# Performance work log

Hardware: AMD Instinct MI355X
Metric: run time of the kernel (lower is better)

## Reference

```python
import jax, jax.numpy as jnp
import numpy as np

NUM_HEADS = 8
HEAD_DIM = 64
WIN = (8, 8, 8)  # (wT, wH, wW)


def setup_inputs() -> dict:
    key = jax.random.key(0)
    k1, k2, k3 = jax.random.split(key, 3)
    B, T, H, W, C = 2, 16, 32, 32, 512
    d_inner = NUM_HEADS * HEAD_DIM  # 512
    x = jax.random.normal(k1, (B, T * H * W, C), dtype=jnp.float32)
    # torch Linear weights stored transposed as [in, out] for y = x @ w
    w_qkv = jax.random.normal(k2, (C, 3 * d_inner), dtype=jnp.float32) * (C ** -0.5)
    w_proj = jax.random.normal(k3, (d_inner, C), dtype=jnp.float32) * (d_inner ** -0.5)
    b_proj = jnp.zeros((C,), dtype=jnp.float32)
    return {"x": x, "w_qkv": w_qkv, "w_proj": w_proj, "b_proj": b_proj,
            "T": T, "H": H, "W": W}


def reference(x, w_qkv, w_proj, b_proj, T, H, W):
    B, N, C = x.shape
    wT, wH, wW = WIN
    scale = HEAD_DIM ** -0.5
    # module re-derives T if N mismatches T*H*W
    if N != T * H * W:
        T = N // (H * W)
    xv = x.reshape(B, T, H, W, C)
    pt, ph, pw = (-T) % wT, (-H) % wH, (-W) % wW
    if pt or ph or pw:
        xv = jnp.pad(xv, ((0, 0), (0, pt), (0, ph), (0, pw), (0, 0)))
    Tp, Hp, Wp = T + pt, H + ph, W + pw
    nT, nH, nW = Tp // wT, Hp // wH, Wp // wW
    L = wT * wH * wW  # tokens per window
    # window partition: [B*nT*nH*nW, L, C]
    xw = xv.reshape(B, nT, wT, nH, wH, nW, wW, C)
    xw = xw.transpose(0, 1, 3, 5, 2, 4, 6, 7).reshape(-1, L, C)
    # qkv projection (no bias)
    qkv = xw @ w_qkv  # [nw, L, 3*nh*hd]
    q, k, v = jnp.split(qkv, 3, axis=-1)

    def heads(t):
        return t.reshape(t.shape[0], L, NUM_HEADS, HEAD_DIM).transpose(0, 2, 1, 3)

    q, k, v = heads(q), heads(k), heads(v)  # [nw, h, L, d]
    attn = jax.nn.softmax(jnp.einsum('nhid,nhjd->nhij', q, k) * scale, axis=-1)
    o = jnp.einsum('nhij,nhjd->nhid', attn, v)
    o = o.transpose(0, 2, 1, 3).reshape(-1, L, NUM_HEADS * HEAD_DIM)
    o = o @ w_proj + b_proj  # output projection
    # window un-partition
    o = o.reshape(B, nT, nH, nW, wT, wH, wW, C)
    o = o.transpose(0, 1, 4, 2, 5, 3, 6, 7).reshape(B, Tp, Hp, Wp, C)
    return o[:, :T, :H, :W].reshape(B, N, C)
```

## Files before the change

### kernel.cpp

```cpp
#include <hip/hip_runtime.h>
#include <hip/hip_bf16.h>

typedef __hip_bfloat16 bf16;
typedef __attribute__((ext_vector_type(8))) short bf16x8;
typedef __attribute__((ext_vector_type(4))) float f32x4;

#define MROWS 32768
#define CDIM 512
#define SEL_STRIDE (512*512*64)

__device__ __forceinline__ int win_to_src_row(int m) {
  int win = m >> 9, l = m & 511;
  int b = win >> 5, rr = win & 31;
  int nt = rr >> 4, nh = (rr >> 2) & 3, nw = rr & 3;
  int wt = l >> 6, wh = (l >> 3) & 7, ww = l & 7;
  int tt = nt * 8 + wt, hh = nh * 8 + wh, wp = nw * 8 + ww;
  return (b << 14) + (tt << 10) + (hh << 5) + wp;
}

__device__ __forceinline__ unsigned short bf16bits(bf16 h) {
  return __builtin_bit_cast(unsigned short, h);
}

__device__ __forceinline__ ushort4 pack4(f32x4 a) {
  ushort4 o;
  o.x = bf16bits(__float2bfloat16(a[0]));
  o.y = bf16bits(__float2bfloat16(a[1]));
  o.z = bf16bits(__float2bfloat16(a[2]));
  o.w = bf16bits(__float2bfloat16(a[3]));
  return o;
}

__device__ __forceinline__ int xcd_chunk(int bx, int n) {
  return (bx & 7) * (n >> 3) + (bx >> 3);
}

__global__ __launch_bounds__(256) void transpose_cvt_kernel(
    const float* __restrict__ src, bf16* __restrict__ dst, int R, int C) {
  __shared__ float tile[32][33];
  int bc = blockIdx.x * 32, br = blockIdx.y * 32;
  int tx = threadIdx.x, ty = threadIdx.y;
#pragma unroll
  for (int i = 0; i < 32; i += 8)
    tile[ty + i][tx] = src[(size_t)(br + ty + i) * C + bc + tx];
  __syncthreads();
#pragma unroll
  for (int i = 0; i < 32; i += 8)
    dst[(size_t)(bc + ty + i) * R + br + tx] = __float2bfloat16(tile[tx][ty + i]);
}

__global__ __launch_bounds__(256) void perm_x_kernel(const float* __restrict__ x,
                                                     bf16* __restrict__ xw) {
  const int total = MROWS * (CDIM / 4);
  for (int i = blockIdx.x * 256 + threadIdx.x; i < total; i += 2048 * 256) {
    int m = i >> 7, c4 = (i & 127) * 4;
    int src = win_to_src_row(m);
    float4 v = *(const float4*)(x + (size_t)src * CDIM + c4);
    ushort4 o;
    o.x = bf16bits(__float2bfloat16(v.x));
    o.y = bf16bits(__float2bfloat16(v.y));
    o.z = bf16bits(__float2bfloat16(v.z));
    o.w = bf16bits(__float2bfloat16(v.w));
    *(ushort4*)(xw + (size_t)m * CDIM + c4) = o;
  }
}

#define BM 128
#define BN 128
#define BK 64

__device__ __forceinline__ void gload16(const bf16* g, const bf16* l) {
  __builtin_amdgcn_global_load_lds(
      (const __attribute__((address_space(1))) unsigned int*)g,
      (__attribute__((address_space(3))) unsigned int*)l, 16, 0, 0);
}

template <int MODE, int SWAP>
__global__ __launch_bounds__(256) void gemm_bt_kernel(
    const bf16* __restrict__ A, const bf16* __restrict__ Bt, int Ntiles, int bn0,
    bf16* __restrict__ qkv_out, float* __restrict__ out,
    const float* __restrict__ bias) {
  __shared__ __align__(16) bf16 Asl[BM * BK];
  __shared__ __align__(16) bf16 Bsl[BN * BK];
  const int K = 512;
  int l2 = xcd_chunk(blockIdx.x, gridDim.x);
  int bn = bn0 + (l2 >> 3) % Ntiles;
  int bm = (l2 & 7) + (l2 / (8 * Ntiles)) * 8;
  int t = threadIdx.x, lane = t & 63, w = t >> 6;
  int wr = w >> 1, wc = w & 1;
  int l15 = lane & 15, lh = lane >> 4;
  f32x4 acc[4][4] = {};

  for (int kt = 0; kt < K; kt += BK) {
    __syncthreads();
#pragma unroll
    for (int i = 0; i < 4; ++i) {
      int f = i * 256 + t;
      int row = f >> 3, cb = f & 7;
      gload16(A + (size_t)(bm * BM + row) * K + kt + cb * 8,
              &Asl[(i * 256 + w * 64) * 8]);
    }
#pragma unroll
    for (int i = 0; i < 4; ++i) {
      int f = i * 256 + t;
      int row = f >> 3, cb = f & 7;
      gload16(Bt + (size_t)(bn * BN + row) * K + kt + cb * 8,
              &Bsl[(i * 256 + w * 64) * 8]);
    }
    __syncthreads();
#pragma unroll
    for (int kk = 0; kk < 2; ++kk) {
      bf16x8 af[4], bfr[4];
#pragma unroll
      for (int mi = 0; mi < 4; ++mi)
        af[mi] = *(const bf16x8*)&Asl[(wr * 64 + mi * 16 + l15) * BK + kk * 32 + lh * 8];
#pragma unroll
      for (int nj = 0; nj < 4; ++nj)
        bfr[nj] = *(const bf16x8*)&Bsl[(wc * 64 + nj * 16 + l15) * BK + kk * 32 + lh * 8];
#pragma unroll
      for (int mi = 0; mi < 4; ++mi)
#pragma unroll
        for (int nj = 0; nj < 4; ++nj) {
          if (SWAP)
            acc[mi][nj] = __builtin_amdgcn_mfma_f32_16x16x32_bf16(
                bfr[nj], af[mi], acc[mi][nj], 0, 0, 0);
          else
            acc[mi][nj] = __builtin_amdgcn_mfma_f32_16x16x32_bf16(
                af[mi], bfr[nj], acc[mi][nj], 0, 0, 0);
        }
    }
  }

  if (MODE == 0 && SWAP == 1) {
#pragma unroll
    for (int mi = 0; mi < 4; ++mi) {
      int tok_g = bm * BM + wr * 64 + mi * 16 + l15;
      int win = tok_g >> 9, tk = tok_g & 511;
#pragma unroll
      for (int nj = 0; nj < 4; ++nj) {
        int c = bn * BN + wc * 64 + nj * 16 + lh * 4;
        int sel = c >> 9, cc = c & 511;
        int head = cc >> 6, d0 = cc & 63;
        *(ushort4*)(qkv_out + (size_t)sel * SEL_STRIDE +
                    (((size_t)(win * 8 + head)) * 512 + tk) * 64 + d0) =
            pack4(acc[mi][nj]);
      }
    }
  } else if (MODE == 0) {
#pragma unroll
    for (int mi = 0; mi < 4; ++mi) {
      int tok0 = bm * BM + wr * 64 + mi * 16 + lh * 4;
      int win = tok0 >> 9, tk0 = tok0 & 511;
#pragma unroll
      for (int nj = 0; nj < 4; ++nj) {
        int cc = (bn - 8) * BN + wc * 64 + nj * 16 + l15;
        int head = cc >> 6, d = cc & 63;
        *(ushort4*)(qkv_out + 2 * (size_t)SEL_STRIDE +
                    (((size_t)(win * 8 + head)) * 64 + d) * 512 + tk0) =
            pack4(acc[mi][nj]);
      }
    }
  } else {
#pragma unroll
    for (int mi = 0; mi < 4; ++mi) {
      int row = bm * BM + wr * 64 + mi * 16 + lh * 4;
#pragma unroll
      for (int r = 0; r < 4; ++r) {
        int srow = win_to_src_row(row + r);
        float* op = out + (size_t)srow * CDIM;
#pragma unroll
        for (int nj = 0; nj < 4; ++nj) {
          int col = bn * BN + wc * 64 + nj * 16 + l15;
          op[col] = acc[mi][nj][r] + bias[col];
        }
      }
    }
  }
}

__global__ __launch_bounds__(256, 2) void attn_kernel(const bf16* __restrict__ qkv_ws,
                                                      bf16* __restrict__ o_ws) {
  __shared__ __align__(16) bf16 Pl[4][4][16 * 64];
  int l2 = xcd_chunk(blockIdx.x, 1024);
  int wh = l2 >> 1, qc = l2 & 1;
  int win = wh >> 3, head = wh & 7;
  int t = threadIdx.x, lane = t & 63, w = t >> 6;
  int l15 = lane & 15, lh = lane >> 4;
  const bf16* qb = qkv_ws + (size_t)wh * (512 * 64);
  const bf16* kb = qb + SEL_STRIDE;
  const bf16* vtb = qkv_ws + 2 * (size_t)SEL_STRIDE + (size_t)wh * (64 * 512);

  const float c_scale = 0.18033688011112042f;
  int q0 = qc * 256 + w * 64;
  bf16x8 qf[4][2];
#pragma unroll
  for (int qi = 0; qi < 4; ++qi)
#pragma unroll
    for (int kk = 0; kk < 2; ++kk)
      qf[qi][kk] = *(const bf16x8*)(qb + (size_t)(q0 + qi * 16 + l15) * 64 + kk * 32 + lh * 8);

  f32x4 acco[4][4] = {};
  float lsum[4][4] = {};
  for (int kt = 0; kt < 8; ++kt) {
    bf16x8 kf[4][2], vf[4][2];
#pragma unroll
    for (int kj = 0; kj < 4; ++kj) {
      int tok = kt * 64 + kj * 16 + l15;
#pragma unroll
      for (int kk = 0; kk < 2; ++kk)
        kf[kj][kk] = *(const bf16x8*)(kb + (size_t)tok * 64 + kk * 32 + lh * 8);
    }
#pragma unroll
    for (int nj = 0; nj < 4; ++nj) {
      int d = nj * 16 + l15;
#pragma unroll
      for (int kk = 0; kk < 2; ++kk)
        vf[nj][kk] = *(const bf16x8*)(vtb + (size_t)d * 512 + kt * 64 + kk * 32 + lh * 8);
    }
#pragma unroll
    for (int qi = 0; qi < 4; ++qi) {
      f32x4 s[4] = {};
#pragma unroll
      for (int kj = 0; kj < 4; ++kj)
#pragma unroll
        for (int kk = 0; kk < 2; ++kk)
          s[kj] = __builtin_amdgcn_mfma_f32_16x16x32_bf16(qf[qi][kk], kf[kj][kk], s[kj], 0, 0, 0);
#pragma unroll
      for (int kj = 0; kj < 4; ++kj)
#pragma unroll
        for (int r = 0; r < 4; ++r) {
          float p = __builtin_exp2f(s[kj][r] * c_scale);
          s[kj][r] = p;
          lsum[qi][r] += p;
        }
      char* myP = (char*)&Pl[w][qi][0];
#pragma unroll
      for (int kj = 0; kj < 4; ++kj)
#pragma unroll
        for (int r = 0; r < 4; ++r) {
          int prow = lh * 4 + r, pcol = kj * 16 + l15;
          *(bf16*)(myP + prow * 128 + ((pcol * 2) ^ ((prow & 7) << 4))) =
              __float2bfloat16(s[kj][r]);
        }
      bf16x8 pa[2];
#pragma unroll
      for (int kk = 0; kk < 2; ++kk)
        pa[kk] = *(const bf16x8*)(myP + l15 * 128 + ((kk * 64 + lh * 16) ^ ((l15 & 7) << 4)));
#pragma unroll
      for (int nj = 0; nj < 4; ++nj)
#pragma unroll
        for (int kk = 0; kk < 2; ++kk)
          acco[qi][nj] = __builtin_amdgcn_mfma_f32_16x16x32_bf16(pa[kk], vf[nj][kk],
                                                                 acco[qi][nj], 0, 0, 0);
    }
  }
#pragma unroll
  for (int qi = 0; qi < 4; ++qi) {
    float inv[4];
#pragma unroll
    for (int r = 0; r < 4; ++r) {
      float v = lsum[qi][r];
      v += __shfl_xor(v, 1);
      v += __shfl_xor(v, 2);
      v += __shfl_xor(v, 4);
      v += __shfl_xor(v, 8);
      inv[r] = __frcp_rn(v);
    }
#pragma unroll
    for (int nj = 0; nj < 4; ++nj)
#pragma unroll
      for (int r = 0; r < 4; ++r) {
        int row = q0 + qi * 16 + lh * 4 + r;
        int d = nj * 16 + l15;
        o_ws[((size_t)win * 512 + row) * 512 + head * 64 + d] =
            __float2bfloat16(acco[qi][nj][r] * inv[r]);
      }
  }
}

extern "C" void kernel_launch(void* const* d_in, const int* in_sizes, int n_in,
                              void* d_out, int out_size, void* d_ws, size_t ws_size,
                              hipStream_t stream) {
  const float* x = (const float*)d_in[0];
  const float* w_qkv = (const float*)d_in[1];
  const float* w_proj = (const float*)d_in[2];
  const float* b_proj = (const float*)d_in[3];
  float* out = (float*)d_out;

  const size_t OFF_QKV = 33554432;
  const size_t OFF_WQ = OFF_QKV + 100663296;
  const size_t OFF_WP = OFF_WQ + 1572864;
  const size_t NEED = OFF_WP + 524288;
  if (ws_size < NEED) return;

  char* ws = (char*)d_ws;
  bf16* xw = (bf16*)ws;
  bf16* qkv = (bf16*)(ws + OFF_QKV);
  bf16* wqkvT = (bf16*)(ws + OFF_WQ);
  bf16* wprojT = (bf16*)(ws + OFF_WP);
  bf16* o_ws = xw;

  transpose_cvt_kernel<<<dim3(1536 / 32, 512 / 32), dim3(32, 8), 0, stream>>>(w_qkv, wqkvT, 512, 1536);
  transpose_cvt_kernel<<<dim3(512 / 32, 512 / 32), dim3(32, 8), 0, stream>>>(w_proj, wprojT, 512, 512);
  perm_x_kernel<<<2048, 256, 0, stream>>>(x, xw);
  gemm_bt_kernel<0, 1><<<256 * 8, 256, 0, stream>>>(xw, wqkvT, 8, 0, qkv, nullptr, nullptr);
  gemm_bt_kernel<0, 0><<<256 * 4, 256, 0, stream>>>(xw, wqkvT, 4, 8, qkv, nullptr, nullptr);
  attn_kernel<<<1024, 256, 0, stream>>>(qkv, o_ws);
  gemm_bt_kernel<1, 0><<<256 * 4, 256, 0, stream>>>(o_ws, wprojT, 4, 0, nullptr, out, b_proj);
}
```

Measured before the change: 240.1 us.

## Keep attention probabilities in registers, merge QKV GEMM launches, vectorize projection stores

The attention kernel now computes S transposed (K as the A operand) in 32-key chunks. It packs the probabilities to bf16 with v_cvt_pk_bf16_f32 and rearranges them across lanes with ds_bpermute, replacing the LDS round trip for P. The per-row softmax sum is reduced with fewer shuffles. The two QKV GEMM launches are merged into one launch of 12 column tiles, with a runtime branch choosing the operand order and epilogue. The output projection is switched to the swapped layout so it can write float4 rows and load bias as vectors. This adds permute instructions and a divergence-free runtime branch in the GEMM, and halves the key-chunk size, which creates more loop iterations.

New measurement: 237.7 us. About the same (-1.0%).

```diff
diff --git a/kernel.cpp b/kernel.cpp
--- a/kernel.cpp
+++ b/kernel.cpp
@@ -4,6 +4,7 @@
 typedef __hip_bfloat16 bf16;
 typedef __attribute__((ext_vector_type(8))) short bf16x8;
 typedef __attribute__((ext_vector_type(4))) float f32x4;
+typedef __attribute__((ext_vector_type(4))) unsigned int u32x4;
 
 #define MROWS 32768
 #define CDIM 512
@@ -29,6 +30,12 @@
   o.z = bf16bits(__float2bfloat16(a[2]));
   o.w = bf16bits(__float2bfloat16(a[3]));
   return o;
+}
+
+__device__ __forceinline__ unsigned int cvtpk_bf16(float lo, float hi) {
+  unsigned int r;
+  asm("v_cvt_pk_bf16_f32 %0, %1, %2" : "=v"(r) : "v"(lo), "v"(hi));
+  return r;
 }
 
 __device__ __forceinline__ int xcd_chunk(int bx, int n) {
@@ -75,20 +82,21 @@
       (__attribute__((address_space(3))) unsigned int*)l, 16, 0, 0);
 }
 
-template <int MODE, int SWAP>
+template <int MODE>
 __global__ __launch_bounds__(256) void gemm_bt_kernel(
-    const bf16* __restrict__ A, const bf16* __restrict__ Bt, int Ntiles, int bn0,
+    const bf16* __restrict__ A, const bf16* __restrict__ Bt, int Ntiles,
     bf16* __restrict__ qkv_out, float* __restrict__ out,
     const float* __restrict__ bias) {
   __shared__ __align__(16) bf16 Asl[BM * BK];
   __shared__ __align__(16) bf16 Bsl[BN * BK];
   const int K = 512;
   int l2 = xcd_chunk(blockIdx.x, gridDim.x);
-  int bn = bn0 + (l2 >> 3) % Ntiles;
+  int bn = (l2 >> 3) % Ntiles;
   int bm = (l2 & 7) + (l2 / (8 * Ntiles)) * 8;
   int t = threadIdx.x, lane = t & 63, w = t >> 6;
   int wr = w >> 1, wc = w & 1;
   int l15 = lane & 15, lh = lane >> 4;
+  const bool swp = (MODE == 1) || (bn < 8);
   f32x4 acc[4][4] = {};
 
   for (int kt = 0; kt < K; kt += BK) {
@@ -108,71 +116,90 @@
               &Bsl[(i * 256 + w * 64) * 8]);
     }
     __syncthreads();
-#pragma unroll
-    for (int kk = 0; kk < 2; ++kk) {
-      bf16x8 af[4], bfr[4];
-#pragma unroll
-      for (int mi = 0; mi < 4; ++mi)
-        af[mi] = *(const bf16x8*)&Asl[(wr * 64 + mi * 16 + l15) * BK + kk * 32 + lh * 8];
-#pragma unroll
-      for (int nj = 0; nj < 4; ++nj)
-        bfr[nj] = *(const bf16x8*)&Bsl[(wc * 64 + nj * 16 + l15) * BK + kk * 32 + lh * 8];
-#pragma unroll
-      for (int mi = 0; mi < 4; ++mi)
-#pragma unroll
-        for (int nj = 0; nj < 4; ++nj) {
-          if (SWAP)
+    if (swp) {
+#pragma unroll
+      for (int kk = 0; kk < 2; ++kk) {
+        bf16x8 af[4], bfr[4];
+#pragma unroll
+        for (int mi = 0; mi < 4; ++mi)
+          af[mi] = *(const bf16x8*)&Asl[(wr * 64 + mi * 16 + l15) * BK + kk * 32 + lh * 8];
+#pragma unroll
+        for (int nj = 0; nj < 4; ++nj)
+          bfr[nj] = *(const bf16x8*)&Bsl[(wc * 64 + nj * 16 + l15) * BK + kk * 32 + lh * 8];
+#pragma unroll
+        for (int mi = 0; mi < 4; ++mi)
+#pragma unroll
+          for (int nj = 0; nj < 4; ++nj)
             acc[mi][nj] = __builtin_amdgcn_mfma_f32_16x16x32_bf16(
                 bfr[nj], af[mi], acc[mi][nj], 0, 0, 0);
-          else
+      }
+    } else {
+#pragma unroll
+      for (int kk = 0; kk < 2; ++kk) {
+        bf16x8 af[4], bfr[4];
+#pragma unroll
+        for (int mi = 0; mi < 4; ++mi)
+          af[mi] = *(const bf16x8*)&Asl[(wr * 64 + mi * 16 + l15) * BK + kk * 32 + lh * 8];
+#pragma unroll
+        for (int nj = 0; nj < 4; ++nj)
+          bfr[nj] = *(const bf16x8*)&Bsl[(wc * 64 + nj * 16 + l15) * BK + kk * 32 + lh * 8];
+#pragma unroll
+        for (int mi = 0; mi < 4; ++mi)
+#pragma unroll
+          for (int nj = 0; nj < 4; ++nj)
             acc[mi][nj] = __builtin_amdgcn_mfma_f32_16x16x32_bf16(
                 af[mi], bfr[nj], acc[mi][nj], 0, 0, 0);
+      }
+    }
+  }
+
+  if (MODE == 0) {
+    if (bn < 8) {
+#pragma unroll
+      for (int mi = 0; mi < 4; ++mi) {
+        int tok_g = bm * BM + wr * 64 + mi * 16 + l15;
+        int win = tok_g >> 9, tk = tok_g & 511;
+#pragma unroll
+        for (int nj = 0; nj < 4; ++nj) {
+          int c = bn * BN + wc * 64 + nj * 16 + lh * 4;
+          int sel = c >> 9, cc = c & 511;
+          int head = cc >> 6, d0 = cc & 63;
+          *(ushort4*)(qkv_out + (size_t)sel * SEL_STRIDE +
+                      (((size_t)(win * 8 + head)) * 512 + tk) * 64 + d0) =
+              pack4(acc[mi][nj]);
         }
-    }
-  }
-
-  if (MODE == 0 && SWAP == 1) {
+      }
+    } else {
+#pragma unroll
+      for (int mi = 0; mi < 4; ++mi) {
+        int tok0 = bm * BM + wr * 64 + mi * 16 + lh * 4;
+        int win = tok0 >> 9, tk0 = tok0 & 511;
+#pragma unroll
+        for (int nj = 0; nj < 4; ++nj) {
+          int cc = (bn - 8) * BN + wc * 64 + nj * 16 + l15;
+          int head = cc >> 6, d = cc & 63;
+          *(ushort4*)(qkv_out + 2 * (size_t)SEL_STRIDE +
+                      (((size_t)(win * 8 + head)) * 64 + d) * 512 + tk0) =
+              pack4(acc[mi][nj]);
+        }
+      }
+    }
+  } else {
 #pragma unroll
     for (int mi = 0; mi < 4; ++mi) {
-      int tok_g = bm * BM + wr * 64 + mi * 16 + l15;
-      int win = tok_g >> 9, tk = tok_g & 511;
+      int row = bm * BM + wr * 64 + mi * 16 + l15;
+      int srow = win_to_src_row(row);
+      float* op = out + (size_t)srow * CDIM;
 #pragma unroll
       for (int nj = 0; nj < 4; ++nj) {
-        int c = bn * BN + wc * 64 + nj * 16 + lh * 4;
-        int sel = c >> 9, cc = c & 511;
-        int head = cc >> 6, d0 = cc & 63;
-        *(ushort4*)(qkv_out + (size_t)sel * SEL_STRIDE +
-                    (((size_t)(win * 8 + head)) * 512 + tk) * 64 + d0) =
-            pack4(acc[mi][nj]);
-      }
-    }
-  } else if (MODE == 0) {
-#pragma unroll
-    for (int mi = 0; mi < 4; ++mi) {
-      int tok0 = bm * BM + wr * 64 + mi * 16 + lh * 4;
-      int win = tok0 >> 9, tk0 = tok0 & 511;
-#pragma unroll
-      for (int nj = 0; nj < 4; ++nj) {
-        int cc = (bn - 8) * BN + wc * 64 + nj * 16 + l15;
-        int head = cc >> 6, d = cc & 63;
-        *(ushort4*)(qkv_out + 2 * (size_t)SEL_STRIDE +
-                    (((size_t)(win * 8 + head)) * 64 + d) * 512 + tk0) =
-            pack4(acc[mi][nj]);
-      }
-    }
-  } else {
-#pragma unroll
-    for (int mi = 0; mi < 4; ++mi) {
-      int row = bm * BM + wr * 64 + mi * 16 + lh * 4;
-#pragma unroll
-      for (int r = 0; r < 4; ++r) {
-        int srow = win_to_src_row(row + r);
-        float* op = out + (size_t)srow * CDIM;
-#pragma unroll
-        for (int nj = 0; nj < 4; ++nj) {
-          int col = bn * BN + wc * 64 + nj * 16 + l15;
-          op[col] = acc[mi][nj][r] + bias[col];
-        }
+        int col = bn * BN + wc * 64 + nj * 16 + lh * 4;
+        float4 bv = *(const float4*)(bias + col);
+        float4 v;
+        v.x = acc[mi][nj][0] + bv.x;
+        v.y = acc[mi][nj][1] + bv.y;
+        v.z = acc[mi][nj][2] + bv.z;
+        v.w = acc[mi][nj][3] + bv.w;
+        *(float4*)(op + col) = v;
       }
     }
   }
@@ -180,7 +207,6 @@
 
 __global__ __launch_bounds__(256, 2) void attn_kernel(const bf16* __restrict__ qkv_ws,
                                                       bf16* __restrict__ o_ws) {
-  __shared__ __align__(16) bf16 Pl[4][4][16 * 64];
   int l2 = xcd_chunk(blockIdx.x, 1024);
   int wh = l2 >> 1, qc = l2 & 1;
   int win = wh >> 3, head = wh & 7;
@@ -199,73 +225,70 @@
     for (int kk = 0; kk < 2; ++kk)
       qf[qi][kk] = *(const bf16x8*)(qb + (size_t)(q0 + qi * 16 + l15) * 64 + kk * 32 + lh * 8);
 
+  int idx0 = (((((2 * lh + 0) & 3) << 4) + l15) << 2);
+  int idx1 = (((((2 * lh + 1) & 3) << 4) + l15) << 2);
+  int kjsel = lh >> 1;
+
   f32x4 acco[4][4] = {};
-  float lsum[4][4] = {};
-  for (int kt = 0; kt < 8; ++kt) {
-    bf16x8 kf[4][2], vf[4][2];
-#pragma unroll
-    for (int kj = 0; kj < 4; ++kj) {
-      int tok = kt * 64 + kj * 16 + l15;
+  float lsum[4] = {0.f, 0.f, 0.f, 0.f};
+  for (int ck = 0; ck < 16; ++ck) {
+    bf16x8 kf[2][2], vf[4];
+#pragma unroll
+    for (int kj = 0; kj < 2; ++kj) {
+      int tok = ck * 32 + kj * 16 + l15;
 #pragma unroll
       for (int kk = 0; kk < 2; ++kk)
         kf[kj][kk] = *(const bf16x8*)(kb + (size_t)tok * 64 + kk * 32 + lh * 8);
     }
 #pragma unroll
-    for (int nj = 0; nj < 4; ++nj) {
-      int d = nj * 16 + l15;
-#pragma unroll
-      for (int kk = 0; kk < 2; ++kk)
-        vf[nj][kk] = *(const bf16x8*)(vtb + (size_t)d * 512 + kt * 64 + kk * 32 + lh * 8);
-    }
+    for (int nj = 0; nj < 4; ++nj)
+      vf[nj] = *(const bf16x8*)(vtb + (size_t)(nj * 16 + l15) * 512 + ck * 32 + lh * 8);
 #pragma unroll
     for (int qi = 0; qi < 4; ++qi) {
-      f32x4 s[4] = {};
-#pragma unroll
-      for (int kj = 0; kj < 4; ++kj)
-#pragma unroll
-        for (int kk = 0; kk < 2; ++kk)
-          s[kj] = __builtin_amdgcn_mfma_f32_16x16x32_bf16(qf[qi][kk], kf[kj][kk], s[kj], 0, 0, 0);
-#pragma unroll
-      for (int kj = 0; kj < 4; ++kj)
-#pragma unroll
-        for (int r = 0; r < 4; ++r) {
-          float p = __builtin_exp2f(s[kj][r] * c_scale);
-          s[kj][r] = p;
-          lsum[qi][r] += p;
-        }
-      char* myP = (char*)&Pl[w][qi][0];
-#pragma unroll
-      for (int kj = 0; kj < 4; ++kj)
-#pragma unroll
-        for (int r = 0; r < 4; ++r) {
-          int prow = lh * 4 + r, pcol = kj * 16 + l15;
-          *(bf16*)(myP + prow * 128 + ((pcol * 2) ^ ((prow & 7) << 4))) =
-              __float2bfloat16(s[kj][r]);
-        }
-      bf16x8 pa[2];
-#pragma unroll
-      for (int kk = 0; kk < 2; ++kk)
-        pa[kk] = *(const bf16x8*)(myP + l15 * 128 + ((kk * 64 + lh * 16) ^ ((l15 & 7) << 4)));
+      f32x4 s0 = {}, s1 = {};
+#pragma unroll
+      for (int kk = 0; kk < 2; ++kk) {
+        s0 = __builtin_amdgcn_mfma_f32_16x16x32_bf16(kf[0][kk], qf[qi][kk], s0, 0, 0, 0);
+        s1 = __builtin_amdgcn_mfma_f32_16x16x32_bf16(kf[1][kk], qf[qi][kk], s1, 0, 0, 0);
+      }
+      float p00 = __builtin_exp2f(s0[0] * c_scale);
+      float p01 = __builtin_exp2f(s0[1] * c_scale);
+      float p02 = __builtin_exp2f(s0[2] * c_scale);
+      float p03 = __builtin_exp2f(s0[3] * c_scale);
+      float p10 = __builtin_exp2f(s1[0] * c_scale);
+      float p11 = __builtin_exp2f(s1[1] * c_scale);
+      float p12 = __builtin_exp2f(s1[2] * c_scale);
+      float p13 = __builtin_exp2f(s1[3] * c_scale);
+      lsum[qi] += ((p00 + p01) + (p02 + p03)) + ((p10 + p11) + (p12 + p13));
+      unsigned int pk00 = cvtpk_bf16(p00, p01), pk01 = cvtpk_bf16(p02, p03);
+      unsigned int pk10 = cvtpk_bf16(p10, p11), pk11 = cvtpk_bf16(p12, p13);
+      unsigned int a0 = (unsigned int)__builtin_amdgcn_ds_bpermute(idx0, (int)pk00);
+      unsigned int b0 = (unsigned int)__builtin_amdgcn_ds_bpermute(idx0, (int)pk10);
+      unsigned int a1 = (unsigned int)__builtin_amdgcn_ds_bpermute(idx0, (int)pk01);
+      unsigned int b1 = (unsigned int)__builtin_amdgcn_ds_bpermute(idx0, (int)pk11);
+      unsigned int a2 = (unsigned int)__builtin_amdgcn_ds_bpermute(idx1, (int)pk00);
+      unsigned int b2 = (unsigned int)__builtin_amdgcn_ds_bpermute(idx1, (int)pk10);
+      unsigned int a3 = (unsigned int)__builtin_amdgcn_ds_bpermute(idx1, (int)pk01);
+      unsigned int b3 = (unsigned int)__builtin_amdgcn_ds_bpermute(idx1, (int)pk11);
+      u32x4 pu;
+      pu[0] = kjsel ? b0 : a0;
+      pu[1] = kjsel ? b1 : a1;
+      pu[2] = kjsel ? b2 : a2;
+      pu[3] = kjsel ? b3 : a3;
+      bf16x8 pa = __builtin_bit_cast(bf16x8, pu);
 #pragma unroll
       for (int nj = 0; nj < 4; ++nj)
-#pragma unroll
-        for (int kk = 0; kk < 2; ++kk)
-          acco[qi][nj] = __builtin_amdgcn_mfma_f32_16x16x32_bf16(pa[kk], vf[nj][kk],
-                                                                 acco[qi][nj], 0, 0, 0);
+        acco[qi][nj] = __builtin_amdgcn_mfma_f32_16x16x32_bf16(pa, vf[nj], acco[qi][nj], 0, 0, 0);
     }
   }
 #pragma unroll
   for (int qi = 0; qi < 4; ++qi) {
+    float v = lsum[qi];
+    v += __shfl_xor(v, 16);
+    v += __shfl_xor(v, 32);
     float inv[4];
 #pragma unroll
-    for (int r = 0; r < 4; ++r) {
-      float v = lsum[qi][r];
-      v += __shfl_xor(v, 1);
-      v += __shfl_xor(v, 2);
-      v += __shfl_xor(v, 4);
-      v += __shfl_xor(v, 8);
-      inv[r] = __frcp_rn(v);
-    }
+    for (int r = 0; r < 4; ++r) inv[r] = __frcp_rn(__shfl(v, lh * 4 + r));
 #pragma unroll
     for (int nj = 0; nj < 4; ++nj)
 #pragma unroll
@@ -303,8 +326,7 @@
   transpose_cvt_kernel<<<dim3(1536 / 32, 512 / 32), dim3(32, 8), 0, stream>>>(w_qkv, wqkvT, 512, 1536);
   transpose_cvt_kernel<<<dim3(512 / 32, 512 / 32), dim3(32, 8), 0, stream>>>(w_proj, wprojT, 512, 512);
   perm_x_kernel<<<2048, 256, 0, stream>>>(x, xw);
-  gemm_bt_kernel<0, 1><<<256 * 8, 256, 0, stream>>>(xw, wqkvT, 8, 0, qkv, nullptr, nullptr);
-  gemm_bt_kernel<0, 0><<<256 * 4, 256, 0, stream>>>(xw, wqkvT, 4, 8, qkv, nullptr, nullptr);
+  gemm_bt_kernel<0><<<256 * 12, 256, 0, stream>>>(xw, wqkvT, 12, qkv, nullptr, nullptr);
   attn_kernel<<<1024, 256, 0, stream>>>(qkv, o_ws);
-  gemm_bt_kernel<1, 0><<<256 * 4, 256, 0, stream>>>(o_ws, wprojT, 4, 0, nullptr, out, b_proj);
-}
+  gemm_bt_kernel<1><<<256 * 4, 256, 0, stream>>>(o_ws, wprojT, 4, nullptr, out, b_proj);
+}
```
